# Optimization experiments

Measured on AMD Instinct MI355X. Metric: run time of the kernel, lower is better.

The kernel has to match this reference:

```python
import jax, jax.numpy as jnp
import numpy as np

N_NODES = 50000
N_EDGES = 600000
D = 128
N_GRAPHS = 64


def setup_inputs() -> dict:
    key = jax.random.key(0)
    ks = jax.random.split(key, 16)
    x = jax.random.normal(ks[0], (N_NODES, D), dtype=jnp.float32)
    edge_index = jax.random.randint(ks[1], (2, N_EDGES), 0, N_NODES, dtype=jnp.int64)
    batch = jnp.sort(jax.random.randint(ks[2], (N_NODES,), 0, N_GRAPHS, dtype=jnp.int64))
    s = 1.0 / np.sqrt(D)
    def lin(k, out_d, in_d):
        return jax.random.uniform(k, (out_d, in_d), jnp.float32, -s, s)
    inp = {"x": x, "edge_index": edge_index, "batch": batch}
    for i, base in zip(range(3), (3, 6, 9)):
        inp[f"W_rel{i+1}"] = lin(ks[base], D, D)
        inp[f"b_rel{i+1}"] = jax.random.uniform(ks[base + 1], (D,), jnp.float32, -s, s)
        inp[f"W_root{i+1}"] = lin(ks[base + 2], D, D)
    s5 = 1.0 / np.sqrt(5)
    inp["W1"] = lin(ks[12], 5, D)
    inp["b1"] = jax.random.uniform(ks[13], (5,), jnp.float32, -s, s)
    inp["W2"] = jax.random.uniform(ks[14], (1, 5), jnp.float32, -s5, s5)
    inp["b2"] = jax.random.uniform(ks[15], (1,), jnp.float32, -s5, s5)
    return inp


def graph_conv(x, src, dst, W_rel, b_rel, W_root):
    # PyG GraphConv: out_i = W_root x_i + W_rel * sum_{j->i} x_j + b_rel
    agg = jax.ops.segment_sum(x[src], dst, num_segments=N_NODES)  # [N, D]
    return agg @ W_rel.T + b_rel + x @ W_root.T


def reference(x, edge_index, batch,
              W_rel1, b_rel1, W_root1,
              W_rel2, b_rel2, W_root2,
              W_rel3, b_rel3, W_root3,
              W1, b1, W2, b2):
    src, dst = edge_index[0], edge_index[1]
    h = jax.nn.relu(graph_conv(x, src, dst, W_rel1, b_rel1, W_root1))
    h = jax.nn.relu(graph_conv(h, src, dst, W_rel2, b_rel2, W_root2))
    h = graph_conv(h, src, dst, W_rel3, b_rel3, W_root3)
    # global max pool over graphs
    g = jax.ops.segment_max(h, batch, num_segments=N_GRAPHS)  # [G, D]
    out = jax.nn.relu(g @ W1.T + b1) @ W2.T + b2  # [G, 1]
    return out
```

## Files before the change

### kernel.cpp

```cpp
#include <hip/hip_runtime.h>
#include <float.h>

#define N_NODES 50000
#define N_EDGES 600000
#define D 128
#define N_GRAPHS 64
#define SCAN_T 256
#define SCAN_NBLK ((N_NODES + SCAN_T - 1) / SCAN_T)

typedef __attribute__((ext_vector_type(8))) short short8;
typedef __attribute__((ext_vector_type(4))) float floatx4;

__device__ inline float bf2f(unsigned short h) {
    return __uint_as_float((unsigned)h << 16);
}
__device__ inline unsigned short f2bf(float f) {
    unsigned u = __float_as_uint(f);
    return (unsigned short)((u + 0x7fffu + ((u >> 16) & 1u)) >> 16);
}


__device__ inline void acc8v(int2 u, float ss, float* a) {
    a[0] += (float)(signed char)(u.x      ) * ss;
    a[1] += (float)(signed char)(u.x >>  8) * ss;
    a[2] += (float)(signed char)(u.x >> 16) * ss;
    a[3] += (float)(u.x >> 24)              * ss;
    a[4] += (float)(signed char)(u.y      ) * ss;
    a[5] += (float)(signed char)(u.y >>  8) * ss;
    a[6] += (float)(signed char)(u.y >> 16) * ss;
    a[7] += (float)(u.y >> 24)              * ss;
}

__device__ inline short8 deq8(int2 u, float ss) {
    short8 r;
    r[0] = (short)f2bf((float)(signed char)(u.x      ) * ss);
    r[1] = (short)f2bf((float)(signed char)(u.x >>  8) * ss);
    r[2] = (short)f2bf((float)(signed char)(u.x >> 16) * ss);
    r[3] = (short)f2bf((float)(u.x >> 24)              * ss);
    r[4] = (short)f2bf((float)(signed char)(u.y      ) * ss);
    r[5] = (short)f2bf((float)(signed char)(u.y >>  8) * ss);
    r[6] = (short)f2bf((float)(signed char)(u.y >> 16) * ss);
    r[7] = (short)f2bf((float)(u.y >> 24)              * ss);
    return r;
}


__global__ __launch_bounds__(256) void cast_prep(
    const float* __restrict__ x,
    signed char* __restrict__ xq, float* __restrict__ xs,
    const float* __restrict__ Wr0, const float* __restrict__ Wo0,
    const float* __restrict__ Wr1, const float* __restrict__ Wo1,
    const float* __restrict__ Wr2, const float* __restrict__ Wo2,
    unsigned short* __restrict__ B0, unsigned short* __restrict__ B1,
    unsigned short* __restrict__ B2,
    int* __restrict__ deg, float* __restrict__ g)
{
    int t = blockIdx.x * 256 + threadIdx.x;
    if (t < N_NODES * 16) {
        int node = t >> 4, ln = t & 15;
        const float4* xr = (const float4*)(x + (size_t)node * D + ln * 8);
        float4 v0 = xr[0], v1 = xr[1];
        float v[8] = {v0.x, v0.y, v0.z, v0.w, v1.x, v1.y, v1.z, v1.w};
        float am = 0.f;
#pragma unroll
        for (int i = 0; i < 8; ++i) am = fmaxf(am, fabsf(v[i]));
#pragma unroll
        for (int m = 1; m < 16; m <<= 1) am = fmaxf(am, __shfl_xor(am, m, 16));
        float inv = (am > 0.f) ? 127.f / am : 0.f;
        int q0 = 0, q1 = 0;
#pragma unroll
        for (int i = 0; i < 4; ++i) { int q = (int)rintf(v[i]     * inv); q0 |= (q & 0xff) << (8 * i); }
#pragma unroll
        for (int i = 0; i < 4; ++i) { int q = (int)rintf(v[4 + i] * inv); q1 |= (q & 0xff) << (8 * i); }
        int2 qp; qp.x = q0; qp.y = q1;
        *(int2*)(xq + (size_t)node * D + ln * 8) = qp;
        if (ln == 0) xs[node] = am * (1.f / 127.f);
        return;
    }
    int w = t - N_NODES * 16;
    if (w < 3 * 128 * 256) {
        int l = w >> 15;
        int r = w & 32767;
        int o = r >> 8, k = r & 255;
        const float* Wr = (l == 0) ? Wr0 : (l == 1) ? Wr1 : Wr2;
        const float* Wo = (l == 0) ? Wo0 : (l == 1) ? Wo1 : Wo2;
        unsigned short* B = (l == 0) ? B0 : (l == 1) ? B1 : B2;
        float v = (k < 128) ? Wr[o * 128 + k] : Wo[o * 128 + (k - 128)];
        B[r] = f2bf(v);
        return;
    }
    w -= 3 * 128 * 256;
    if (w < N_NODES) { deg[w] = 0; return; }
    w -= N_NODES;
    if (w < N_GRAPHS * D) g[w] = -FLT_MAX;
}


__global__ void count_deg(const int* __restrict__ ei, int* __restrict__ deg) {
    int e = blockIdx.x * 256 + threadIdx.x;
    if (e < N_EDGES) atomicAdd(&deg[ei[N_EDGES + e]], 1);
}

__global__ __launch_bounds__(SCAN_T) void block_sum(const int* __restrict__ deg,
                                                    int* __restrict__ blockSums) {
    __shared__ int s[SCAN_T];
    int tid = threadIdx.x;
    int i = blockIdx.x * SCAN_T + tid;
    s[tid] = (i < N_NODES) ? deg[i] : 0;
    __syncthreads();
    for (int off = SCAN_T / 2; off > 0; off >>= 1) {
        if (tid < off) s[tid] += s[tid + off];
        __syncthreads();
    }
    if (tid == 0) blockSums[blockIdx.x] = s[0];
}

__global__ __launch_bounds__(SCAN_T) void scan_write(const int* __restrict__ deg,
                                                     const int* __restrict__ blockSums,
                                                     int* __restrict__ row_start,
                                                     int* __restrict__ cursor) {
    __shared__ int bs[SCAN_T];
    __shared__ int s[SCAN_T];
    int tid = threadIdx.x;
    bs[tid] = (tid < SCAN_NBLK) ? blockSums[tid] : 0;
    __syncthreads();
    for (int off = 1; off < SCAN_T; off <<= 1) {
        int tt = (tid >= off) ? bs[tid - off] : 0;
        __syncthreads();
        bs[tid] += tt;
        __syncthreads();
    }
    int myOff = (blockIdx.x == 0) ? 0 : bs[blockIdx.x - 1];
    if (blockIdx.x == 0 && tid == SCAN_T - 1) row_start[N_NODES] = bs[tid];

    int i = blockIdx.x * SCAN_T + tid;
    int v = (i < N_NODES) ? deg[i] : 0;
    s[tid] = v;
    __syncthreads();
    for (int off = 1; off < SCAN_T; off <<= 1) {
        int tt = (tid >= off) ? s[tid - off] : 0;
        __syncthreads();
        s[tid] += tt;
        __syncthreads();
    }
    if (i < N_NODES) {
        int rs = myOff + s[tid] - v;
        row_start[i] = rs;
        cursor[i]    = rs;
    }
}

__global__ void fill_csr(const int* __restrict__ ei, int* __restrict__ cursor,
                         int* __restrict__ csr_src) {
    int e = blockIdx.x * 256 + threadIdx.x;
    if (e < N_EDGES) {
        int dst = ei[N_EDGES + e];
        int pos = atomicAdd(&cursor[dst], 1);
        csr_src[pos] = ei[e];
    }
}


__device__ inline void gather_frag(const signed char* __restrict__ xq,
                                   const float* __restrict__ xs,
                                   const int* __restrict__ row_start,
                                   const int* __restrict__ csr_src,
                                   int node, int m, int quad, float* a)
{
#pragma unroll
    for (int i = 0; i < 32; ++i) a[i] = 0.f;
    if (node >= N_NODES) return;
    int beg = row_start[node];
    int end = row_start[node + 1];
    for (int base = beg; base < end; base += 4) {
        int n = end - base; if (n > 4) n = 4;
        int idx = (quad < n) ? csr_src[base + quad] : 0;
        for (int j = 0; j < n; ++j) {
            int s = __shfl(idx, m + 16 * j, 64);
            const signed char* rp = xq + (size_t)s * D + quad * 8;
            int2 q0 = *(const int2*)(rp);
            int2 q1 = *(const int2*)(rp + 32);
            int2 q2 = *(const int2*)(rp + 64);
            int2 q3 = *(const int2*)(rp + 96);
            float ss = xs[s];
            acc8v(q0, ss, a); acc8v(q1, ss, a + 8);
            acc8v(q2, ss, a + 16); acc8v(q3, ss, a + 24);
        }
    }
}


__device__ inline void stage_b_half(unsigned short* sB, const unsigned short* __restrict__ Bb,
                                    int tid, int h) {
#pragma unroll
    for (int i = 0; i < 8; ++i) {
        int flat = tid + i * 256;
        int fi = flat >> 6, ln = flat & 63;
        int mm = ln & 15, qq = ln >> 4;
        int ksL = fi >> 3, tt = fi & 7;
        short8 v = *(const short8*)(Bb + (size_t)(tt * 16 + mm) * 256
                                    + (h * 4 + ksL) * 32 + qq * 8);
        *(short8*)(sB + (size_t)flat * 8) = v;
    }
}


struct GemmShared {
    union {
        unsigned short b[16384];
        float c[64 * 130];
    };
};

__global__ __launch_bounds__(256) void layer_fused(
    const signed char* __restrict__ xq, const float* __restrict__ xs,
    const int* __restrict__ row_start, const int* __restrict__ csr_src,
    const unsigned short* __restrict__ Bb, const float* __restrict__ bias,
    signed char* __restrict__ Oq, float* __restrict__ Os)
{
    __shared__ GemmShared sh;
    int tid  = threadIdx.x;
    int wave = tid >> 6;
    int lane = tid & 63;
    int m    = lane & 15;
    int quad = lane >> 4;
    int row0 = blockIdx.x * 64 + wave * 16;
    int node = row0 + m;

    float a[32];
    gather_frag(xq, xs, row_start, csr_src, node, m, quad, a);

    short8 afA[4];
#pragma unroll
    for (int ks = 0; ks < 4; ++ks) {
        short8 f;
#pragma unroll
        for (int j = 0; j < 8; ++j) f[j] = (short)f2bf(a[ks * 8 + j]);
        afA[ks] = f;
    }

    int arow = (node < N_NODES) ? node : N_NODES - 1;
    const signed char* xr = xq + (size_t)arow * D + quad * 8;
    float fsr = xs[arow];
    short8 afX[4];
    afX[0] = deq8(*(const int2*)(xr),      fsr);
    afX[1] = deq8(*(const int2*)(xr + 32), fsr);
    afX[2] = deq8(*(const int2*)(xr + 64), fsr);
    afX[3] = deq8(*(const int2*)(xr + 96), fsr);

    floatx4 acc[8];
#pragma unroll
    for (int t = 0; t < 8; ++t) acc[t] = (floatx4){0.f, 0.f, 0.f, 0.f};

    stage_b_half(sh.b, Bb, tid, 0);
    __syncthreads();
#pragma unroll
    for (int ksL = 0; ksL < 4; ++ksL)
#pragma unroll
        for (int t = 0; t < 8; ++t) {
            short8 b = *(const short8*)(sh.b + (size_t)((ksL * 8 + t) * 64 + lane) * 8);
            acc[t] = __builtin_amdgcn_mfma_f32_16x16x32_bf16(afA[ksL], b, acc[t], 0, 0, 0);
        }
    __syncthreads();
    stage_b_half(sh.b, Bb, tid, 1);
    __syncthreads();
#pragma unroll
    for (int ksL = 0; ksL < 4; ++ksL)
#pragma unroll
        for (int t = 0; t < 8; ++t) {
            short8 b = *(const short8*)(sh.b + (size_t)((ksL * 8 + t) * 64 + lane) * 8);
            acc[t] = __builtin_amdgcn_mfma_f32_16x16x32_bf16(afX[ksL], b, acc[t], 0, 0, 0);
        }
    __syncthreads();

#pragma unroll
    for (int t = 0; t < 8; ++t) {
        int col = t * 16 + m;
        float bv = bias[col];
#pragma unroll
        for (int r = 0; r < 4; ++r)
            sh.c[(wave * 16 + quad * 4 + r) * 130 + col] = fmaxf(acc[t][r] + bv, 0.f);
    }
    __syncthreads();

    int lr  = tid >> 2;
    int seg = tid & 3;
    int grow = blockIdx.x * 64 + lr;
    const float* cp = &sh.c[lr * 130 + seg * 32];
    float vv[32];
    float am = 0.f;
#pragma unroll
    for (int i = 0; i < 32; ++i) { vv[i] = cp[i]; am = fmaxf(am, fabsf(vv[i])); }
    am = fmaxf(am, __shfl_xor(am, 1));
    am = fmaxf(am, __shfl_xor(am, 2));
    float inv = (am > 0.f) ? 127.f / am : 0.f;

    if (grow < N_NODES) {
        int qd[8];
#pragma unroll
        for (int d = 0; d < 8; ++d) {
            int q = 0;
#pragma unroll
            for (int i = 0; i < 4; ++i) {
                int qq = (int)rintf(vv[d * 4 + i] * inv);
                q |= (qq & 0xff) << (8 * i);
            }
            qd[d] = q;
        }
        int4 p0; p0.x = qd[0]; p0.y = qd[1]; p0.z = qd[2]; p0.w = qd[3];
        int4 p1; p1.x = qd[4]; p1.y = qd[5]; p1.z = qd[6]; p1.w = qd[7];
        *(int4*)(Oq + (size_t)grow * 128 + seg * 32)      = p0;
        *(int4*)(Oq + (size_t)grow * 128 + seg * 32 + 16) = p1;
        if (seg == 0) Os[grow] = am * (1.f / 127.f);
    }
}


struct PoolShared {
    union {
        unsigned short b[16384];
        float c[64 * 129];
    };
};

__global__ __launch_bounds__(256) void layer_pool(
    const signed char* __restrict__ xq, const float* __restrict__ xs,
    const int* __restrict__ row_start, const int* __restrict__ csr_src,
    const unsigned short* __restrict__ Bb, const float* __restrict__ bias,
    const int* __restrict__ batch, float* __restrict__ g)
{
    __shared__ PoolShared sh;
    __shared__ int bl[64];
    int tid  = threadIdx.x;
    int wave = tid >> 6;
    int lane = tid & 63;
    int m    = lane & 15;
    int quad = lane >> 4;
    int row0 = blockIdx.x * 64;
    int node = row0 + wave * 16 + m;

    float a[32];
    gather_frag(xq, xs, row_start, csr_src, node, m, quad, a);

    short8 afA[4];
#pragma unroll
    for (int ks = 0; ks < 4; ++ks) {
        short8 f;
#pragma unroll
        for (int j = 0; j < 8; ++j) f[j] = (short)f2bf(a[ks * 8 + j]);
        afA[ks] = f;
    }

    int arow = (node < N_NODES) ? node : N_NODES - 1;
    const signed char* xr = xq + (size_t)arow * D + quad * 8;
    float fsr = xs[arow];
    short8 afX[4];
    afX[0] = deq8(*(const int2*)(xr),      fsr);
    afX[1] = deq8(*(const int2*)(xr + 32), fsr);
    afX[2] = deq8(*(const int2*)(xr + 64), fsr);
    afX[3] = deq8(*(const int2*)(xr + 96), fsr);

    floatx4 acc[8];
#pragma unroll
    for (int t = 0; t < 8; ++t) acc[t] = (floatx4){0.f, 0.f, 0.f, 0.f};

    if (tid < 64) {
        int grow = row0 + tid;
        bl[tid] = (grow < N_NODES) ? batch[grow] : -1;
    }
    stage_b_half(sh.b, Bb, tid, 0);
    __syncthreads();
#pragma unroll
    for (int ksL = 0; ksL < 4; ++ksL)
#pragma unroll
        for (int t = 0; t < 8; ++t) {
            short8 b = *(const short8*)(sh.b + (size_t)((ksL * 8 + t) * 64 + lane) * 8);
            acc[t] = __builtin_amdgcn_mfma_f32_16x16x32_bf16(afA[ksL], b, acc[t], 0, 0, 0);
        }
    __syncthreads();
    stage_b_half(sh.b, Bb, tid, 1);
    __syncthreads();
#pragma unroll
    for (int ksL = 0; ksL < 4; ++ksL)
#pragma unroll
        for (int t = 0; t < 8; ++t) {
            short8 b = *(const short8*)(sh.b + (size_t)((ksL * 8 + t) * 64 + lane) * 8);
            acc[t] = __builtin_amdgcn_mfma_f32_16x16x32_bf16(afX[ksL], b, acc[t], 0, 0, 0);
        }
    __syncthreads();

#pragma unroll
    for (int t = 0; t < 8; ++t) {
        int col = t * 16 + m;
        float bv = bias[col];
#pragma unroll
        for (int r = 0; r < 4; ++r)
            sh.c[(wave * 16 + quad * 4 + r) * 129 + col] = acc[t][r] + bv;
    }
    __syncthreads();

    int nvalid = min(64, N_NODES - row0);
    int b0 = bl[0], b1 = bl[nvalid - 1];
    int col  = tid & 127;
    int rbeg = (tid >> 7) * 32;
    for (int gg = b0; gg <= b1; ++gg) {
        float cur = -FLT_MAX;
#pragma unroll
        for (int r = 0; r < 32; ++r) {
            int rr = rbeg + r;
            float v = (bl[rr] == gg) ? sh.c[rr * 129 + col] : -FLT_MAX;
            cur = fmaxf(cur, v);
        }
        if (cur > -FLT_MAX) {
            float* ad = &g[gg * D + col];
            if (cur >= 0.f) atomicMax((int*)ad, __float_as_int(cur));
            else            atomicMin((unsigned int*)ad, __float_as_uint(cur));
        }
    }
}


__global__ __launch_bounds__(64) void mlp_head(const float* __restrict__ g,
                         const float* __restrict__ W1, const float* __restrict__ b1,
                         const float* __restrict__ W2, const float* __restrict__ b2,
                         float* __restrict__ out) {
    int gi = blockIdx.x;
    int lane = threadIdx.x;
    float x0 = g[gi * D + lane];
    float x1 = g[gi * D + 64 + lane];
    float o = b2[0];
#pragma unroll
    for (int j = 0; j < 5; ++j) {
        float p = x0 * W1[j * D + lane] + x1 * W1[j * D + 64 + lane];
#pragma unroll
        for (int off = 32; off > 0; off >>= 1) p += __shfl_xor(p, off, 64);
        o += fmaxf(p + b1[j], 0.f) * W2[j];
    }
    if (lane == 0) out[gi] = o;
}

extern "C" void kernel_launch(void* const* d_in, const int* in_sizes, int n_in,
                              void* d_out, int out_size, void* d_ws, size_t ws_size,
                              hipStream_t stream) {
    const float* x     = (const float*)d_in[0];
    const int*   ei    = (const int*)d_in[1];
    const int*   batch = (const int*)d_in[2];
    const float* Wrel[3]  = {(const float*)d_in[3], (const float*)d_in[6], (const float*)d_in[9]};
    const float* brel[3]  = {(const float*)d_in[4], (const float*)d_in[7], (const float*)d_in[10]};
    const float* Wroot[3] = {(const float*)d_in[5], (const float*)d_in[8], (const float*)d_in[11]};
    const float* W1 = (const float*)d_in[12];
    const float* b1 = (const float*)d_in[13];
    const float* W2 = (const float*)d_in[14];
    const float* b2 = (const float*)d_in[15];
    float* out = (float*)d_out;

    char* ws = (char*)d_ws;
    const size_t nodeB8 = (size_t)N_NODES * D;
    signed char* xq  = (signed char*)(ws);
    signed char* h1q = (signed char*)(ws + 1 * nodeB8);
    signed char* h2q = (signed char*)(ws + 2 * nodeB8);
    char* p = ws + 3 * nodeB8;
    float* xs  = (float*)p;  p += N_NODES * sizeof(float);
    float* h1s = (float*)p;  p += N_NODES * sizeof(float);
    float* h2s = (float*)p;  p += N_NODES * sizeof(float);
    unsigned short* Bb0 = (unsigned short*)p;   p += 128 * 256 * sizeof(unsigned short);
    unsigned short* Bb1 = (unsigned short*)p;   p += 128 * 256 * sizeof(unsigned short);
    unsigned short* Bb2 = (unsigned short*)p;   p += 128 * 256 * sizeof(unsigned short);
    float* g        = (float*)p;                p += N_GRAPHS * D * sizeof(float);
    int*   deg      = (int*)p;                  p += N_NODES * sizeof(int);
    int*   row_start= (int*)p;                  p += (N_NODES + 1) * sizeof(int);
    int*   cursor   = (int*)p;                  p += N_NODES * sizeof(int);
    int*   csr_src  = (int*)p;                  p += N_EDGES * sizeof(int);
    int*   blockSums= (int*)p;                  p += SCAN_NBLK * sizeof(int);

    const int cast_total = N_NODES * 16 + 3 * 128 * 256 + N_NODES + N_GRAPHS * D;
    cast_prep<<<(cast_total + 255) / 256, 256, 0, stream>>>(
        x, xq, xs,
        Wrel[0], Wroot[0], Wrel[1], Wroot[1], Wrel[2], Wroot[2],
        Bb0, Bb1, Bb2, deg, g);

    count_deg<<<(N_EDGES + 255) / 256, 256, 0, stream>>>(ei, deg);
    block_sum<<<SCAN_NBLK, SCAN_T, 0, stream>>>(deg, blockSums);
    scan_write<<<SCAN_NBLK, SCAN_T, 0, stream>>>(deg, blockSums, row_start, cursor);
    fill_csr<<<(N_EDGES + 255) / 256, 256, 0, stream>>>(ei, cursor, csr_src);

    const int mgrid = (N_NODES + 63) / 64;

    layer_fused<<<mgrid, 256, 0, stream>>>(xq,  xs,  row_start, csr_src, Bb0, brel[0], h1q, h1s);
    layer_fused<<<mgrid, 256, 0, stream>>>(h1q, h1s, row_start, csr_src, Bb1, brel[1], h2q, h2s);
    layer_pool <<<mgrid, 256, 0, stream>>>(h2q, h2s, row_start, csr_src, Bb2, brel[2], batch, g);

    mlp_head<<<N_GRAPHS, 64, 0, stream>>>(g, W1, b1, W2, b2, out);
}
```

Measured before the change: 338.8 us.

## Split gather from GEMM and gather per 64-column feature half

Measured after the change: 347.2 us. 1.02x slower.

```diff
diff --git a/kernel.cpp b/kernel.cpp
--- a/kernel.cpp
+++ b/kernel.cpp
@@ -47,7 +47,8 @@
 
 __global__ __launch_bounds__(256) void cast_prep(
     const float* __restrict__ x,
-    signed char* __restrict__ xq, float* __restrict__ xs,
+    signed char* __restrict__ xq0, signed char* __restrict__ xq1,
+    float* __restrict__ xs,
     const float* __restrict__ Wr0, const float* __restrict__ Wo0,
     const float* __restrict__ Wr1, const float* __restrict__ Wo1,
     const float* __restrict__ Wr2, const float* __restrict__ Wo2,
@@ -73,7 +74,8 @@
 #pragma unroll
         for (int i = 0; i < 4; ++i) { int q = (int)rintf(v[4 + i] * inv); q1 |= (q & 0xff) << (8 * i); }
         int2 qp; qp.x = q0; qp.y = q1;
-        *(int2*)(xq + (size_t)node * D + ln * 8) = qp;
+        signed char* dst = (ln < 8) ? xq0 : xq1;
+        *(int2*)(dst + (size_t)node * 64 + (ln & 7) * 8) = qp;
         if (ln == 0) xs[node] = am * (1.f / 127.f);
         return;
     }
@@ -161,32 +163,65 @@
 }
 
 
-__device__ inline void gather_frag(const signed char* __restrict__ xq,
-                                   const float* __restrict__ xs,
-                                   const int* __restrict__ row_start,
-                                   const int* __restrict__ csr_src,
-                                   int node, int m, int quad, float* a)
+__global__ __launch_bounds__(256) void gather_q64(
+    const signed char* __restrict__ xqh, const float* __restrict__ xs,
+    const int* __restrict__ row_start, const int* __restrict__ csr_src,
+    unsigned short* __restrict__ aggh)
 {
-#pragma unroll
-    for (int i = 0; i < 32; ++i) a[i] = 0.f;
+    int grp  = threadIdx.x >> 3;
+    int ln   = threadIdx.x & 7;
+    int node = blockIdx.x * 32 + grp;
     if (node >= N_NODES) return;
     int beg = row_start[node];
     int end = row_start[node + 1];
-    for (int base = beg; base < end; base += 4) {
-        int n = end - base; if (n > 4) n = 4;
-        int idx = (quad < n) ? csr_src[base + quad] : 0;
-        for (int j = 0; j < n; ++j) {
-            int s = __shfl(idx, m + 16 * j, 64);
-            const signed char* rp = xq + (size_t)s * D + quad * 8;
-            int2 q0 = *(const int2*)(rp);
-            int2 q1 = *(const int2*)(rp + 32);
-            int2 q2 = *(const int2*)(rp + 64);
-            int2 q3 = *(const int2*)(rp + 96);
-            float ss = xs[s];
-            acc8v(q0, ss, a); acc8v(q1, ss, a + 8);
-            acc8v(q2, ss, a + 16); acc8v(q3, ss, a + 24);
-        }
-    }
+
+    float a[8];
+#pragma unroll
+    for (int i = 0; i < 8; ++i) a[i] = 0.f;
+
+    for (int base = beg; base < end; base += 8) {
+        int n = end - base; if (n > 8) n = 8;
+        int idx = (ln < n) ? csr_src[base + ln] : 0;
+        int j = 0;
+        for (; j + 7 < n; j += 8) {
+            int s0 = __shfl(idx, 0, 8); int s1 = __shfl(idx, 1, 8);
+            int s2 = __shfl(idx, 2, 8); int s3 = __shfl(idx, 3, 8);
+            int s4 = __shfl(idx, 4, 8); int s5 = __shfl(idx, 5, 8);
+            int s6 = __shfl(idx, 6, 8); int s7 = __shfl(idx, 7, 8);
+            int2 u0 = *(const int2*)(xqh + (size_t)s0 * 64 + ln * 8);
+            int2 u1 = *(const int2*)(xqh + (size_t)s1 * 64 + ln * 8);
+            int2 u2 = *(const int2*)(xqh + (size_t)s2 * 64 + ln * 8);
+            int2 u3 = *(const int2*)(xqh + (size_t)s3 * 64 + ln * 8);
+            int2 u4 = *(const int2*)(xqh + (size_t)s4 * 64 + ln * 8);
+            int2 u5 = *(const int2*)(xqh + (size_t)s5 * 64 + ln * 8);
+            int2 u6 = *(const int2*)(xqh + (size_t)s6 * 64 + ln * 8);
+            int2 u7 = *(const int2*)(xqh + (size_t)s7 * 64 + ln * 8);
+            float ss0 = xs[s0], ss1 = xs[s1], ss2 = xs[s2], ss3 = xs[s3];
+            float ss4 = xs[s4], ss5 = xs[s5], ss6 = xs[s6], ss7 = xs[s7];
+            acc8v(u0, ss0, a); acc8v(u1, ss1, a); acc8v(u2, ss2, a); acc8v(u3, ss3, a);
+            acc8v(u4, ss4, a); acc8v(u5, ss5, a); acc8v(u6, ss6, a); acc8v(u7, ss7, a);
+        }
+        for (; j + 3 < n; j += 4) {
+            int s0 = __shfl(idx, j,     8); int s1 = __shfl(idx, j + 1, 8);
+            int s2 = __shfl(idx, j + 2, 8); int s3 = __shfl(idx, j + 3, 8);
+            int2 u0 = *(const int2*)(xqh + (size_t)s0 * 64 + ln * 8);
+            int2 u1 = *(const int2*)(xqh + (size_t)s1 * 64 + ln * 8);
+            int2 u2 = *(const int2*)(xqh + (size_t)s2 * 64 + ln * 8);
+            int2 u3 = *(const int2*)(xqh + (size_t)s3 * 64 + ln * 8);
+            float ss0 = xs[s0], ss1 = xs[s1], ss2 = xs[s2], ss3 = xs[s3];
+            acc8v(u0, ss0, a); acc8v(u1, ss1, a); acc8v(u2, ss2, a); acc8v(u3, ss3, a);
+        }
+        for (; j < n; ++j) {
+            int s0 = __shfl(idx, j, 8);
+            int2 u0 = *(const int2*)(xqh + (size_t)s0 * 64 + ln * 8);
+            float ss0 = xs[s0];
+            acc8v(u0, ss0, a);
+        }
+    }
+    short8 r;
+#pragma unroll
+    for (int i = 0; i < 8; ++i) r[i] = (short)f2bf(a[i]);
+    *(short8*)(aggh + (size_t)node * 64 + ln * 8) = r;
 }
 
 
@@ -212,11 +247,13 @@
     };
 };
 
-__global__ __launch_bounds__(256) void layer_fused(
-    const signed char* __restrict__ xq, const float* __restrict__ xs,
-    const int* __restrict__ row_start, const int* __restrict__ csr_src,
+__global__ __launch_bounds__(256) void gemm_mfma(
+    const unsigned short* __restrict__ agg0, const unsigned short* __restrict__ agg1,
+    const signed char* __restrict__ xq0, const signed char* __restrict__ xq1,
+    const float* __restrict__ xs,
     const unsigned short* __restrict__ Bb, const float* __restrict__ bias,
-    signed char* __restrict__ Oq, float* __restrict__ Os)
+    signed char* __restrict__ Oq0, signed char* __restrict__ Oq1,
+    float* __restrict__ Os)
 {
     __shared__ GemmShared sh;
     int tid  = threadIdx.x;
@@ -225,28 +262,24 @@
     int m    = lane & 15;
     int quad = lane >> 4;
     int row0 = blockIdx.x * 64 + wave * 16;
-    int node = row0 + m;
-
-    float a[32];
-    gather_frag(xq, xs, row_start, csr_src, node, m, quad, a);
+
+    int arow = row0 + m;
+    if (arow > N_NODES - 1) arow = N_NODES - 1;
 
     short8 afA[4];
-#pragma unroll
-    for (int ks = 0; ks < 4; ++ks) {
-        short8 f;
-#pragma unroll
-        for (int j = 0; j < 8; ++j) f[j] = (short)f2bf(a[ks * 8 + j]);
-        afA[ks] = f;
-    }
-
-    int arow = (node < N_NODES) ? node : N_NODES - 1;
-    const signed char* xr = xq + (size_t)arow * D + quad * 8;
+    afA[0] = *(const short8*)(agg0 + (size_t)arow * 64 +      quad * 8);
+    afA[1] = *(const short8*)(agg0 + (size_t)arow * 64 + 32 + quad * 8);
+    afA[2] = *(const short8*)(agg1 + (size_t)arow * 64 +      quad * 8);
+    afA[3] = *(const short8*)(agg1 + (size_t)arow * 64 + 32 + quad * 8);
+
     float fsr = xs[arow];
+    const signed char* xr0 = xq0 + (size_t)arow * 64 + quad * 8;
+    const signed char* xr1 = xq1 + (size_t)arow * 64 + quad * 8;
     short8 afX[4];
-    afX[0] = deq8(*(const int2*)(xr),      fsr);
-    afX[1] = deq8(*(const int2*)(xr + 32), fsr);
-    afX[2] = deq8(*(const int2*)(xr + 64), fsr);
-    afX[3] = deq8(*(const int2*)(xr + 96), fsr);
+    afX[0] = deq8(*(const int2*)(xr0),      fsr);
+    afX[1] = deq8(*(const int2*)(xr0 + 32), fsr);
+    afX[2] = deq8(*(const int2*)(xr1),      fsr);
+    afX[3] = deq8(*(const int2*)(xr1 + 32), fsr);
 
     floatx4 acc[8];
 #pragma unroll
@@ -307,10 +340,12 @@
             }
             qd[d] = q;
         }
+        signed char* Oh = (seg < 2) ? Oq0 : Oq1;
+        size_t base = (size_t)grow * 64 + (seg & 1) * 32;
         int4 p0; p0.x = qd[0]; p0.y = qd[1]; p0.z = qd[2]; p0.w = qd[3];
         int4 p1; p1.x = qd[4]; p1.y = qd[5]; p1.z = qd[6]; p1.w = qd[7];
-        *(int4*)(Oq + (size_t)grow * 128 + seg * 32)      = p0;
-        *(int4*)(Oq + (size_t)grow * 128 + seg * 32 + 16) = p1;
+        *(int4*)(Oh + base)      = p0;
+        *(int4*)(Oh + base + 16) = p1;
         if (seg == 0) Os[grow] = am * (1.f / 127.f);
     }
 }
@@ -323,9 +358,10 @@
     };
 };
 
-__global__ __launch_bounds__(256) void layer_pool(
-    const signed char* __restrict__ xq, const float* __restrict__ xs,
-    const int* __restrict__ row_start, const int* __restrict__ csr_src,
+__global__ __launch_bounds__(256) void gemm_pool(
+    const unsigned short* __restrict__ agg0, const unsigned short* __restrict__ agg1,
+    const signed char* __restrict__ xq0, const signed char* __restrict__ xq1,
+    const float* __restrict__ xs,
     const unsigned short* __restrict__ Bb, const float* __restrict__ bias,
     const int* __restrict__ batch, float* __restrict__ g)
 {
@@ -337,28 +373,24 @@
     int m    = lane & 15;
     int quad = lane >> 4;
     int row0 = blockIdx.x * 64;
-    int node = row0 + wave * 16 + m;
-
-    float a[32];
-    gather_frag(xq, xs, row_start, csr_src, node, m, quad, a);
+
+    int arow = row0 + wave * 16 + m;
+    if (arow > N_NODES - 1) arow = N_NODES - 1;
 
     short8 afA[4];
-#pragma unroll
-    for (int ks = 0; ks < 4; ++ks) {
-        short8 f;
-#pragma unroll
-        for (int j = 0; j < 8; ++j) f[j] = (short)f2bf(a[ks * 8 + j]);
-        afA[ks] = f;
-    }
-
-    int arow = (node < N_NODES) ? node : N_NODES - 1;
-    const signed char* xr = xq + (size_t)arow * D + quad * 8;
+    afA[0] = *(const short8*)(agg0 + (size_t)arow * 64 +      quad * 8);
+    afA[1] = *(const short8*)(agg0 + (size_t)arow * 64 + 32 + quad * 8);
+    afA[2] = *(const short8*)(agg1 + (size_t)arow * 64 +      quad * 8);
+    afA[3] = *(const short8*)(agg1 + (size_t)arow * 64 + 32 + quad * 8);
+
     float fsr = xs[arow];
+    const signed char* xr0 = xq0 + (size_t)arow * 64 + quad * 8;
+    const signed char* xr1 = xq1 + (size_t)arow * 64 + quad * 8;
     short8 afX[4];
-    afX[0] = deq8(*(const int2*)(xr),      fsr);
-    afX[1] = deq8(*(const int2*)(xr + 32), fsr);
-    afX[2] = deq8(*(const int2*)(xr + 64), fsr);
-    afX[3] = deq8(*(const int2*)(xr + 96), fsr);
+    afX[0] = deq8(*(const int2*)(xr0),      fsr);
+    afX[1] = deq8(*(const int2*)(xr0 + 32), fsr);
+    afX[2] = deq8(*(const int2*)(xr1),      fsr);
+    afX[3] = deq8(*(const int2*)(xr1 + 32), fsr);
 
     floatx4 acc[8];
 #pragma unroll
@@ -455,11 +487,17 @@
     float* out = (float*)d_out;
 
     char* ws = (char*)d_ws;
-    const size_t nodeB8 = (size_t)N_NODES * D;
-    signed char* xq  = (signed char*)(ws);
-    signed char* h1q = (signed char*)(ws + 1 * nodeB8);
-    signed char* h2q = (signed char*)(ws + 2 * nodeB8);
-    char* p = ws + 3 * nodeB8;
+    const size_t halfQ = (size_t)N_NODES * 64;
+    const size_t halfA = (size_t)N_NODES * 64 * sizeof(unsigned short);
+    signed char* xq0  = (signed char*)(ws);
+    signed char* xq1  = (signed char*)(ws + 1 * halfQ);
+    signed char* h1q0 = (signed char*)(ws + 2 * halfQ);
+    signed char* h1q1 = (signed char*)(ws + 3 * halfQ);
+    signed char* h2q0 = (signed char*)(ws + 4 * halfQ);
+    signed char* h2q1 = (signed char*)(ws + 5 * halfQ);
+    char* p = ws + 6 * halfQ;
+    unsigned short* ag0 = (unsigned short*)p;  p += halfA;
+    unsigned short* ag1 = (unsigned short*)p;  p += halfA;
     float* xs  = (float*)p;  p += N_NODES * sizeof(float);
     float* h1s = (float*)p;  p += N_NODES * sizeof(float);
     float* h2s = (float*)p;  p += N_NODES * sizeof(float);
@@ -475,7 +513,7 @@
 
     const int cast_total = N_NODES * 16 + 3 * 128 * 256 + N_NODES + N_GRAPHS * D;
     cast_prep<<<(cast_total + 255) / 256, 256, 0, stream>>>(
-        x, xq, xs,
+        x, xq0, xq1, xs,
         Wrel[0], Wroot[0], Wrel[1], Wroot[1], Wrel[2], Wroot[2],
         Bb0, Bb1, Bb2, deg, g);
 
@@ -484,11 +522,18 @@
     scan_write<<<SCAN_NBLK, SCAN_T, 0, stream>>>(deg, blockSums, row_start, cursor);
     fill_csr<<<(N_EDGES + 255) / 256, 256, 0, stream>>>(ei, cursor, csr_src);
 
+    const int ggrid = (N_NODES + 31) / 32;
     const int mgrid = (N_NODES + 63) / 64;
 
-    layer_fused<<<mgrid, 256, 0, stream>>>(xq,  xs,  row_start, csr_src, Bb0, brel[0], h1q, h1s);
-    layer_fused<<<mgrid, 256, 0, stream>>>(h1q, h1s, row_start, csr_src, Bb1, brel[1], h2q, h2s);
-    layer_pool <<<mgrid, 256, 0, stream>>>(h2q, h2s, row_start, csr_src, Bb2, brel[2], batch, g);
+    gather_q64<<<ggrid, 256, 0, stream>>>(xq0, xs, row_start, csr_src, ag0);
+    gather_q64<<<ggrid, 256, 0, stream>>>(xq1, xs, row_start, csr_src, ag1);
+    gemm_mfma<<<mgrid, 256, 0, stream>>>(ag0, ag1, xq0, xq1, xs, Bb0, brel[0], h1q0, h1q1, h1s);
+    gather_q64<<<ggrid, 256, 0, stream>>>(h1q0, h1s, row_start, csr_src, ag0);
+    gather_q64<<<ggrid, 256, 0, stream>>>(h1q1, h1s, row_start, csr_src, ag1);
+    gemm_mfma<<<mgrid, 256, 0, stream>>>(ag0, ag1, h1q0, h1q1, h1s, Bb1, brel[1], h2q0, h2q1, h2s);
+    gather_q64<<<ggrid, 256, 0, stream>>>(h2q0, h2s, row_start, csr_src, ag0);
+    gather_q64<<<ggrid, 256, 0, stream>>>(h2q1, h2s, row_start, csr_src, ag1);
+    gemm_pool<<<mgrid, 256, 0, stream>>>(ag0, ag1, h2q0, h2q1, h2s, Bb2, brel[2], batch, g);
 
     mlp_head<<<N_GRAPHS, 64, 0, stream>>>(g, W1, b1, W2, b2, out);
 }
```

## Split neighbor gather into separate kernel with 16-edge batched int4 loads

Applied to the files above, without the earlier changes.

Result: faster. 331.0 us (-2.3%).

```diff
diff --git a/kernel.cpp b/kernel.cpp
--- a/kernel.cpp
+++ b/kernel.cpp
@@ -19,17 +19,24 @@
     return (unsigned short)((u + 0x7fffu + ((u >> 16) & 1u)) >> 16);
 }
 
-
-__device__ inline void acc8v(int2 u, float ss, float* a) {
-    a[0] += (float)(signed char)(u.x      ) * ss;
-    a[1] += (float)(signed char)(u.x >>  8) * ss;
-    a[2] += (float)(signed char)(u.x >> 16) * ss;
-    a[3] += (float)(u.x >> 24)              * ss;
-    a[4] += (float)(signed char)(u.y      ) * ss;
-    a[5] += (float)(signed char)(u.y >>  8) * ss;
-    a[6] += (float)(signed char)(u.y >> 16) * ss;
-    a[7] += (float)(u.y >> 24)              * ss;
-}
+#define ACCQ(u, ss) {                                                            \
+    int w0_ = (u).x, w1_ = (u).y, w2_ = (u).z, w3_ = (u).w;                      \
+    a[ 0] += (float)(signed char)(w0_      ) * (ss);                             \
+    a[ 1] += (float)(signed char)(w0_ >>  8) * (ss);                             \
+    a[ 2] += (float)(signed char)(w0_ >> 16) * (ss);                             \
+    a[ 3] += (float)(w0_ >> 24)              * (ss);                             \
+    a[ 4] += (float)(signed char)(w1_      ) * (ss);                             \
+    a[ 5] += (float)(signed char)(w1_ >>  8) * (ss);                             \
+    a[ 6] += (float)(signed char)(w1_ >> 16) * (ss);                             \
+    a[ 7] += (float)(w1_ >> 24)              * (ss);                             \
+    a[ 8] += (float)(signed char)(w2_      ) * (ss);                             \
+    a[ 9] += (float)(signed char)(w2_ >>  8) * (ss);                             \
+    a[10] += (float)(signed char)(w2_ >> 16) * (ss);                             \
+    a[11] += (float)(w2_ >> 24)              * (ss);                             \
+    a[12] += (float)(signed char)(w3_      ) * (ss);                             \
+    a[13] += (float)(signed char)(w3_ >>  8) * (ss);                             \
+    a[14] += (float)(signed char)(w3_ >> 16) * (ss);                             \
+    a[15] += (float)(w3_ >> 24)              * (ss); }
 
 __device__ inline short8 deq8(int2 u, float ss) {
     short8 r;
@@ -161,32 +168,53 @@
 }
 
 
-__device__ inline void gather_frag(const signed char* __restrict__ xq,
-                                   const float* __restrict__ xs,
-                                   const int* __restrict__ row_start,
-                                   const int* __restrict__ csr_src,
-                                   int node, int m, int quad, float* a)
+__global__ __launch_bounds__(256) void gather_q16(
+    const signed char* __restrict__ xq, const float* __restrict__ xs,
+    const int* __restrict__ row_start, const int* __restrict__ csr_src,
+    unsigned short* __restrict__ aggb)
 {
-#pragma unroll
-    for (int i = 0; i < 32; ++i) a[i] = 0.f;
+    int grp  = threadIdx.x >> 3;
+    int ln   = threadIdx.x & 7;
+    int node = blockIdx.x * 32 + grp;
     if (node >= N_NODES) return;
     int beg = row_start[node];
     int end = row_start[node + 1];
-    for (int base = beg; base < end; base += 4) {
-        int n = end - base; if (n > 4) n = 4;
-        int idx = (quad < n) ? csr_src[base + quad] : 0;
-        for (int j = 0; j < n; ++j) {
-            int s = __shfl(idx, m + 16 * j, 64);
-            const signed char* rp = xq + (size_t)s * D + quad * 8;
-            int2 q0 = *(const int2*)(rp);
-            int2 q1 = *(const int2*)(rp + 32);
-            int2 q2 = *(const int2*)(rp + 64);
-            int2 q3 = *(const int2*)(rp + 96);
-            float ss = xs[s];
-            acc8v(q0, ss, a); acc8v(q1, ss, a + 8);
-            acc8v(q2, ss, a + 16); acc8v(q3, ss, a + 24);
-        }
-    }
+
+    float a[16];
+#pragma unroll
+    for (int i = 0; i < 16; ++i) a[i] = 0.f;
+
+    for (int base = beg; base < end; base += 16) {
+        int last = end - 1;
+        int i0 = base + ln;      if (i0 > last) i0 = last;
+        int i1 = base + 8 + ln;  if (i1 > last) i1 = last;
+        int idx0 = csr_src[i0];
+        int idx1 = csr_src[i1];
+
+        int sidx[16];
+#pragma unroll
+        for (int j = 0; j < 8; ++j) sidx[j]     = __shfl(idx0, j, 8);
+#pragma unroll
+        for (int j = 0; j < 8; ++j) sidx[8 + j] = __shfl(idx1, j, 8);
+
+        int4 u[16];
+#pragma unroll
+        for (int j = 0; j < 16; ++j)
+            u[j] = *(const int4*)(xq + (size_t)sidx[j] * D + ln * 16);
+        float ss[16];
+#pragma unroll
+        for (int j = 0; j < 16; ++j)
+            ss[j] = (base + j < end) ? xs[sidx[j]] : 0.f;
+
+#pragma unroll
+        for (int j = 0; j < 16; ++j) ACCQ(u[j], ss[j]);
+    }
+
+    short8 r0, r1;
+#pragma unroll
+    for (int i = 0; i < 8; ++i) { r0[i] = (short)f2bf(a[i]); r1[i] = (short)f2bf(a[8 + i]); }
+    *(short8*)(aggb + (size_t)node * D + ln * 16)     = r0;
+    *(short8*)(aggb + (size_t)node * D + ln * 16 + 8) = r1;
 }
 
 
@@ -195,8 +223,8 @@
 #pragma unroll
     for (int i = 0; i < 8; ++i) {
         int flat = tid + i * 256;
-        int fi = flat >> 6, ln = flat & 63;
-        int mm = ln & 15, qq = ln >> 4;
+        int fi = flat >> 6, lnn = flat & 63;
+        int mm = lnn & 15, qq = lnn >> 4;
         int ksL = fi >> 3, tt = fi & 7;
         short8 v = *(const short8*)(Bb + (size_t)(tt * 16 + mm) * 256
                                     + (h * 4 + ksL) * 32 + qq * 8);
@@ -212,9 +240,9 @@
     };
 };
 
-__global__ __launch_bounds__(256) void layer_fused(
+__global__ __launch_bounds__(256) void gemm_mfma(
+    const unsigned short* __restrict__ aggb,
     const signed char* __restrict__ xq, const float* __restrict__ xs,
-    const int* __restrict__ row_start, const int* __restrict__ csr_src,
     const unsigned short* __restrict__ Bb, const float* __restrict__ bias,
     signed char* __restrict__ Oq, float* __restrict__ Os)
 {
@@ -225,23 +253,17 @@
     int m    = lane & 15;
     int quad = lane >> 4;
     int row0 = blockIdx.x * 64 + wave * 16;
-    int node = row0 + m;
-
-    float a[32];
-    gather_frag(xq, xs, row_start, csr_src, node, m, quad, a);
+
+    int arow = row0 + m;
+    if (arow > N_NODES - 1) arow = N_NODES - 1;
 
     short8 afA[4];
 #pragma unroll
-    for (int ks = 0; ks < 4; ++ks) {
-        short8 f;
-#pragma unroll
-        for (int j = 0; j < 8; ++j) f[j] = (short)f2bf(a[ks * 8 + j]);
-        afA[ks] = f;
-    }
-
-    int arow = (node < N_NODES) ? node : N_NODES - 1;
-    const signed char* xr = xq + (size_t)arow * D + quad * 8;
+    for (int ks = 0; ks < 4; ++ks)
+        afA[ks] = *(const short8*)(aggb + (size_t)arow * 128 + ks * 32 + quad * 8);
+
     float fsr = xs[arow];
+    const signed char* xr = xq + (size_t)arow * 128 + quad * 8;
     short8 afX[4];
     afX[0] = deq8(*(const int2*)(xr),      fsr);
     afX[1] = deq8(*(const int2*)(xr + 32), fsr);
@@ -323,9 +345,9 @@
     };
 };
 
-__global__ __launch_bounds__(256) void layer_pool(
+__global__ __launch_bounds__(256) void gemm_pool(
+    const unsigned short* __restrict__ aggb,
     const signed char* __restrict__ xq, const float* __restrict__ xs,
-    const int* __restrict__ row_start, const int* __restrict__ csr_src,
     const unsigned short* __restrict__ Bb, const float* __restrict__ bias,
     const int* __restrict__ batch, float* __restrict__ g)
 {
@@ -337,23 +359,17 @@
     int m    = lane & 15;
     int quad = lane >> 4;
     int row0 = blockIdx.x * 64;
-    int node = row0 + wave * 16 + m;
-
-    float a[32];
-    gather_frag(xq, xs, row_start, csr_src, node, m, quad, a);
+
+    int arow = row0 + wave * 16 + m;
+    if (arow > N_NODES - 1) arow = N_NODES - 1;
 
     short8 afA[4];
 #pragma unroll
-    for (int ks = 0; ks < 4; ++ks) {
-        short8 f;
-#pragma unroll
-        for (int j = 0; j < 8; ++j) f[j] = (short)f2bf(a[ks * 8 + j]);
-        afA[ks] = f;
-    }
-
-    int arow = (node < N_NODES) ? node : N_NODES - 1;
-    const signed char* xr = xq + (size_t)arow * D + quad * 8;
+    for (int ks = 0; ks < 4; ++ks)
+        afA[ks] = *(const short8*)(aggb + (size_t)arow * 128 + ks * 32 + quad * 8);
+
     float fsr = xs[arow];
+    const signed char* xr = xq + (size_t)arow * 128 + quad * 8;
     short8 afX[4];
     afX[0] = deq8(*(const int2*)(xr),      fsr);
     afX[1] = deq8(*(const int2*)(xr + 32), fsr);
@@ -460,6 +476,7 @@
     signed char* h1q = (signed char*)(ws + 1 * nodeB8);
     signed char* h2q = (signed char*)(ws + 2 * nodeB8);
     char* p = ws + 3 * nodeB8;
+    unsigned short* aggb = (unsigned short*)p;  p += (size_t)N_NODES * D * sizeof(unsigned short);
     float* xs  = (float*)p;  p += N_NODES * sizeof(float);
     float* h1s = (float*)p;  p += N_NODES * sizeof(float);
     float* h2s = (float*)p;  p += N_NODES * sizeof(float);
@@ -484,11 +501,15 @@
     scan_write<<<SCAN_NBLK, SCAN_T, 0, stream>>>(deg, blockSums, row_start, cursor);
     fill_csr<<<(N_EDGES + 255) / 256, 256, 0, stream>>>(ei, cursor, csr_src);
 
+    const int ggrid = (N_NODES + 31) / 32;
     const int mgrid = (N_NODES + 63) / 64;
 
-    layer_fused<<<mgrid, 256, 0, stream>>>(xq,  xs,  row_start, csr_src, Bb0, brel[0], h1q, h1s);
-    layer_fused<<<mgrid, 256, 0, stream>>>(h1q, h1s, row_start, csr_src, Bb1, brel[1], h2q, h2s);
-    layer_pool <<<mgrid, 256, 0, stream>>>(h2q, h2s, row_start, csr_src, Bb2, brel[2], batch, g);
+    gather_q16<<<ggrid, 256, 0, stream>>>(xq, xs, row_start, csr_src, aggb);
+    gemm_mfma<<<mgrid, 256, 0, stream>>>(aggb, xq, xs, Bb0, brel[0], h1q, h1s);
+    gather_q16<<<ggrid, 256, 0, stream>>>(h1q, h1s, row_start, csr_src, aggb);
+    gemm_mfma<<<mgrid, 256, 0, stream>>>(aggb, h1q, h1s, Bb1, brel[1], h2q, h2s);
+    gather_q16<<<ggrid, 256, 0, stream>>>(h2q, h2s, row_start, csr_src, aggb);
+    gemm_pool<<<mgrid, 256, 0, stream>>>(aggb, h2q, h2s, Bb2, brel[2], batch, g);
 
     mlp_head<<<N_GRAPHS, 64, 0, stream>>>(g, W1, b1, W2, b2, out);
 }
```
